# Kernel optimization log

Hardware: AMD Instinct MI355X
Metric: run time of the kernel (lower is better)

The kernel has to match this reference:

```python
import jax, jax.numpy as jnp
import numpy as np

WS = 4          # window_size
NH = 4          # num_heads
HID = 192       # hidden_dim
IN_DIM = 64     # input_dim
GROUPS = 8      # min(8, hidden_dim)
EPS = 1e-5


def layer_norm(x, g, b):
    mu = jnp.mean(x, axis=-1, keepdims=True)
    var = jnp.var(x, axis=-1, keepdims=True)
    return (x - mu) * jax.lax.rsqrt(var + EPS) * g + b


def group_norm(x, g, b):
    # x: [B, C, H, W], groups over channels
    B, C, H, W = x.shape
    xg = x.reshape(B, GROUPS, C // GROUPS, H, W)
    mu = jnp.mean(xg, axis=(2, 3, 4), keepdims=True)
    var = jnp.var(xg, axis=(2, 3, 4), keepdims=True)
    xn = ((xg - mu) * jax.lax.rsqrt(var + EPS)).reshape(B, C, H, W)
    return xn * g[None, :, None, None] + b[None, :, None, None]


def setup_inputs() -> dict:
    key = jax.random.key(0)
    ks = jax.random.split(key, 16)
    B, H, W = 8, 128, 128
    s = lambda *shape: 0.02
    inp = {
        "x": jax.random.normal(ks[0], (B, IN_DIM, H, W), jnp.float32),
        "h": jax.random.normal(ks[1], (B, HID, H, W), jnp.float32),
        "c": jax.random.normal(ks[2], (B, HID, H, W), jnp.float32),
        # in_proj: Conv2d(input_dim+hidden_dim -> hidden_dim, 1x1)
        "w_in": jax.random.normal(ks[3], (HID, IN_DIM + HID), jnp.float32) * 0.02,
        "b_in": jnp.zeros((HID,), jnp.float32),
        # LocalWindowAttention params
        "ln_g": jnp.ones((HID,), jnp.float32),
        "ln_b": jnp.zeros((HID,), jnp.float32),
        "w_qkv": jax.random.normal(ks[4], (3 * HID, HID), jnp.float32) * 0.02,
        "b_qkv": jnp.zeros((3 * HID,), jnp.float32),
        "w_proj": jax.random.normal(ks[5], (HID, HID), jnp.float32) * 0.02,
        "b_proj": jnp.zeros((HID,), jnp.float32),
        # GroupNorm (shared: applied to attn_map and hnext)
        "gn_g": jnp.ones((HID,), jnp.float32),
        "gn_b": jnp.zeros((HID,), jnp.float32),
        # gates_conv: Conv2d(hidden_dim -> 4*hidden_dim, 1x1)
        "w_gates": jax.random.normal(ks[6], (4 * HID, HID), jnp.float32) * 0.02,
        "b_gates": jnp.zeros((4 * HID,), jnp.float32),
    }
    return inp


def reference(x, h, c, w_in, b_in, ln_g, ln_b, w_qkv, b_qkv,
              w_proj, b_proj, gn_g, gn_b, w_gates, b_gates):
    B, _, H, W = x.shape
    C = HID
    hd = C // NH
    scale = hd ** -0.5

    # in_proj (1x1 conv == channel GEMM)
    comb = jnp.concatenate([x, h], axis=1)
    proj = jnp.einsum('oc,bchw->bohw', w_in, comb) + b_in[None, :, None, None]

    # H, W are multiples of WS -> no reflect padding (matches torch common path)
    nh, nw = H // WS, W // WS
    # window_partition: [B, C, H, W] -> [B*nh*nw, WS*WS, C]
    xw = proj.reshape(B, C, nh, WS, nw, WS).transpose(0, 2, 4, 3, 5, 1)
    xw = xw.reshape(B * nh * nw, WS * WS, C)

    # LocalWindowAttention
    xn = layer_norm(xw, ln_g, ln_b)
    qkv = xn @ w_qkv.T + b_qkv                       # [Bw, N, 3C]
    Bw, N, _ = qkv.shape
    qkv = qkv.reshape(Bw, N, 3, NH, hd)
    q = qkv[:, :, 0].transpose(0, 2, 1, 3)           # [Bw, NH, N, hd]
    k = qkv[:, :, 1].transpose(0, 2, 1, 3)
    v = qkv[:, :, 2].transpose(0, 2, 1, 3)
    attn = jax.nn.softmax(jnp.einsum('bhnd,bhmd->bhnm', q, k) * scale, axis=-1)
    out = jnp.einsum('bhnm,bhmd->bhnd', attn, v)
    out = out.transpose(0, 2, 1, 3).reshape(Bw, N, C)
    out = out @ w_proj.T + b_proj

    # window_unpartition: [B*nh*nw, WS*WS, C] -> [B, C, H, W]
    amap = out.reshape(B, nh, nw, WS, WS, C).transpose(0, 5, 1, 3, 2, 4)
    amap = amap.reshape(B, C, H, W)

    amap = group_norm(amap, gn_g, gn_b)

    # gates (1x1 conv) + LSTM cell math
    gates = jnp.einsum('oc,bchw->bohw', w_gates, amap) + b_gates[None, :, None, None]
    ci, cf, co, cg = jnp.split(gates, 4, axis=1)
    i = jax.nn.sigmoid(ci)
    f = jax.nn.sigmoid(cf)
    o = jax.nn.sigmoid(co)
    g = jnp.tanh(cg)
    cnext = f * c + i * g
    hnext = o * jnp.tanh(cnext)
    hnext = group_norm(hnext, gn_g, gn_b)
    return (hnext, cnext)
```

## Files before the change

kernel.cpp:

```cpp
#include <hip/hip_runtime.h>

#define HW 16384
#define W_IMG 128
#define CH 192
#define CIN 64
#define P_TOT 131072
#define EPS 1e-5f

__device__ __forceinline__ void blockReduce2(float& a, float& b2, float* lds) {
#pragma unroll
  for (int off = 32; off > 0; off >>= 1) {
    a  += __shfl_down(a,  off, 64);
    b2 += __shfl_down(b2, off, 64);
  }
  int wv = threadIdx.x >> 6, ln = threadIdx.x & 63;
  if (ln == 0) { lds[wv] = a; lds[4 + wv] = b2; }
  __syncthreads();
  if (threadIdx.x == 0) {
    a  = lds[0] + lds[1] + lds[2] + lds[3];
    b2 = lds[4] + lds[5] + lds[6] + lds[7];
  }
}

__global__ __launch_bounds__(256) void k0_prep(
    const float* __restrict__ w_g, float* __restrict__ wT)
{
  int idx = blockIdx.x * 256 + threadIdx.x;
  if (idx < 147456) {
    int row = idx / 192, c = idx - row * 192;
    wT[(size_t)c * 768 + row] = w_g[idx];
  }
}

__global__ __launch_bounds__(256) void k3_fused(
    const float* __restrict__ x,  const float* __restrict__ h,
    const float* __restrict__ w_in, const float* __restrict__ b_in,
    const float* __restrict__ ln_g, const float* __restrict__ ln_b,
    const float* __restrict__ w_qkv, const float* __restrict__ b_qkv,
    const float* __restrict__ w_proj, const float* __restrict__ b_proj,
    float* __restrict__ amap)
{
  __shared__ float buf[576 * 16];
  __shared__ float xnb[192 * 16];
  __shared__ float sc[4 * 16 * 16];
  __shared__ float mu_s[16], rs_s[16];
  const int tid = threadIdx.x;
  const int wid = blockIdx.x;
  const int b  = wid >> 10;
  const int wy = (wid >> 5) & 31;
  const int wx = wid & 31;
  const int pix0 = (wy * 4) * W_IMG + wx * 4;

  for (int idx = tid; idx < 1024; idx += 256) {
    int cch = idx >> 2, ty = idx & 3;
    const float* src = (cch < 64)
        ? x + (size_t)(b * CIN + cch) * HW + pix0 + ty * W_IMG
        : h + (size_t)(b * CH + (cch - 64)) * HW + pix0 + ty * W_IMG;
    const float4 v = *(const float4*)src;
    float* d = &buf[cch * 16 + ty * 4];
    d[0] = v.x; d[1] = v.y; d[2] = v.z; d[3] = v.w;
  }
  __syncthreads();

  if (tid < 192) {
    const int j = tid;
    float acc[16];
    float bj = b_in[j];
#pragma unroll
    for (int t = 0; t < 16; ++t) acc[t] = bj;
    const float* wr = w_in + (size_t)j * 256;
#pragma unroll 4
    for (int c = 0; c < 256; ++c) {
      float wv = wr[c];
      const float* xr = &buf[c * 16];
#pragma unroll
      for (int t = 0; t < 16; ++t) acc[t] = fmaf(wv, xr[t], acc[t]);
    }
    float* o = &xnb[j * 16];
#pragma unroll
    for (int t = 0; t < 16; ++t) o[t] = acc[t];
  }
  __syncthreads();

  if (tid < 16) {
    float s = 0.f, s2 = 0.f;
    for (int j = 0; j < 192; ++j) { float v = xnb[j * 16 + tid]; s += v; s2 += v * v; }
    float mu = s * (1.f / 192.f);
    float var = s2 * (1.f / 192.f) - mu * mu;
    mu_s[tid] = mu;
    rs_s[tid] = rsqrtf(fmaxf(var, 0.f) + EPS);
  }
  __syncthreads();

  for (int idx = tid; idx < 3072; idx += 256) {
    int j = idx >> 4, t = idx & 15;
    xnb[idx] = (xnb[idx] - mu_s[t]) * rs_s[t] * ln_g[j] + ln_b[j];
  }
  __syncthreads();

  for (int j = tid; j < 576; j += 256) {
    float acc[16];
    float bj = b_qkv[j];
#pragma unroll
    for (int t = 0; t < 16; ++t) acc[t] = bj;
    const float* wr = w_qkv + (size_t)j * 192;
#pragma unroll 4
    for (int c = 0; c < 192; ++c) {
      float wv = wr[c];
      const float* xr = &xnb[c * 16];
#pragma unroll
      for (int t = 0; t < 16; ++t) acc[t] = fmaf(wv, xr[t], acc[t]);
    }
    float* qr = &buf[j * 16];
#pragma unroll
    for (int t = 0; t < 16; ++t) qr[t] = acc[t];
  }
  __syncthreads();

  const float scale = 0.14433756729740643f;
  for (int q = tid; q < 1024; q += 256) {
    int hh = q >> 8, t1 = (q >> 4) & 15, t2 = q & 15;
    const float* qq = &buf[(hh * 48) * 16 + t1];
    const float* kk = &buf[(192 + hh * 48) * 16 + t2];
    float sv = 0.f;
#pragma unroll
    for (int d = 0; d < 48; ++d) sv = fmaf(qq[d * 16], kk[d * 16], sv);
    sc[q] = sv * scale;
  }
  __syncthreads();

  if (tid < 64) {
    float* row = &sc[tid * 16];
    float m = row[0];
#pragma unroll
    for (int t = 1; t < 16; ++t) m = fmaxf(m, row[t]);
    float sum = 0.f;
#pragma unroll
    for (int t = 0; t < 16; ++t) { float e = __expf(row[t] - m); row[t] = e; sum += e; }
    float inv = 1.f / sum;
#pragma unroll
    for (int t = 0; t < 16; ++t) row[t] *= inv;
  }
  __syncthreads();

  for (int rnd = 0; rnd < 12; ++rnd) {
    int q = rnd * 256 + tid;
    int cc = q >> 4, t = q & 15;
    const float* pr = &sc[(cc / 48) * 256 + t * 16];
    const float* vr = &buf[(384 + cc) * 16];
    float sv = 0.f;
#pragma unroll
    for (int t2 = 0; t2 < 16; ++t2) sv = fmaf(pr[t2], vr[t2], sv);
    xnb[cc * 16 + t] = sv;
  }
  __syncthreads();

  if (tid < 192) {
    const int o = tid;
    float acc[16];
    float bo = b_proj[o];
#pragma unroll
    for (int t = 0; t < 16; ++t) acc[t] = bo;
    const float* wr = w_proj + (size_t)o * 192;
#pragma unroll 4
    for (int c = 0; c < 192; ++c) {
      float wv = wr[c];
      const float* xr = &xnb[c * 16];
#pragma unroll
      for (int t = 0; t < 16; ++t) acc[t] = fmaf(wv, xr[t], acc[t]);
    }
    float* op = amap + (size_t)(b * CH + o) * HW + pix0;
#pragma unroll
    for (int ty = 0; ty < 4; ++ty) {
      *(float4*)(op + ty * W_IMG) =
          make_float4(acc[ty * 4], acc[ty * 4 + 1], acc[ty * 4 + 2], acc[ty * 4 + 3]);
    }
  }
}

__global__ __launch_bounds__(256) void k4_stats(
    const float* __restrict__ src, float* __restrict__ stats)
{
  __shared__ float lds[8];
  int blk = blockIdx.x;
  int chunk = blk & 15, bc = blk >> 4;
  int b = bc / 192, cch = bc % 192;
  const float4 v = *(const float4*)(src + (size_t)bc * HW + chunk * 1024 + threadIdx.x * 4);
  float s  = v.x + v.y + v.z + v.w;
  float s2 = v.x * v.x + v.y * v.y + v.z * v.z + v.w * v.w;
  blockReduce2(s, s2, lds);
  if (threadIdx.x == 0) {
    atomicAdd(&stats[(b * 8 + cch / 24) * 2],     s);
    atomicAdd(&stats[(b * 8 + cch / 24) * 2 + 1], s2);
  }
}

__global__ __launch_bounds__(256) void k4b_scale(
    const float* __restrict__ stats, const float* __restrict__ gn_g,
    const float* __restrict__ gn_b, float* __restrict__ scaleS, float* __restrict__ shiftS)
{
  int idx = blockIdx.x * 256 + threadIdx.x;
  if (idx >= 1536) return;
  int b = idx / 192, cch = idx % 192, g = cch / 24;
  float n = 24.f * HW;
  float mu  = stats[(b * 8 + g) * 2] / n;
  float var = stats[(b * 8 + g) * 2 + 1] / n - mu * mu;
  float rs = rsqrtf(fmaxf(var, 0.f) + EPS);
  float scl = rs * gn_g[cch];
  scaleS[idx] = scl;
  shiftS[idx] = gn_b[cch] - mu * scl;
}

__global__ __launch_bounds__(256) void k6_gates(
    float* __restrict__ outp,
    const float* __restrict__ wT,
    const float* __restrict__ b_g, const float* __restrict__ cin,
    const float* __restrict__ scaleS, const float* __restrict__ shiftS)
{
  __shared__ float tile[192 * 64];
  const int tid = threadIdx.x;
  const int b  = blockIdx.x >> 8;
  const int s0 = (blockIdx.x & 255) * 64;
  float* cout = outp + (size_t)P_TOT * CH;

  for (int idx = tid; idx < 12288; idx += 256) {
    int c = idx >> 6, p = idx & 63;
    float raw = outp[(size_t)(b * CH + c) * HW + s0 + p];
    tile[idx] = fmaf(raw, scaleS[b * CH + c], shiftS[b * CH + c]);
  }
  __syncthreads();

  const int lane = tid & 63;
  const int wv = __builtin_amdgcn_readfirstlane(tid >> 6);

  for (int jg = wv * 6; jg < wv * 6 + 6; ++jg) {
    const int j0 = jg * 8;
    float acc[32];
#pragma unroll
    for (int k = 0; k < 4; ++k)
#pragma unroll
      for (int r = 0; r < 8; ++r) acc[k * 8 + r] = b_g[k * 192 + j0 + r];
#pragma unroll 2
    for (int c = 0; c < 192; ++c) {
      float a = tile[c * 64 + lane];
      const float* wc = wT + (size_t)c * 768 + j0;
#pragma unroll
      for (int k = 0; k < 4; ++k)
#pragma unroll
        for (int r = 0; r < 8; ++r)
          acc[k * 8 + r] = fmaf(a, wc[k * 192 + r], acc[k * 8 + r]);
    }
#pragma unroll
    for (int r = 0; r < 8; ++r) {
      size_t base = (size_t)(b * CH + j0 + r) * HW + s0 + lane;
      float ci = acc[r], cf = acc[8 + r], co = acc[16 + r], cg = acc[24 + r];
      float iv = 1.f / (1.f + __expf(-ci));
      float fv = 1.f / (1.f + __expf(-cf));
      float ov = 1.f / (1.f + __expf(-co));
      float gv = 1.f - 2.f / (__expf(2.f * cg) + 1.f);
      float cn = fmaf(fv, cin[base], iv * gv);
      cout[base] = cn;
      float th = 1.f - 2.f / (__expf(2.f * cn) + 1.f);
      outp[base] = ov * th;
    }
  }
}

__global__ __launch_bounds__(256) void k7_hnext(
    const float* __restrict__ stats2,
    const float* __restrict__ gn_g, const float* __restrict__ gn_b,
    float* __restrict__ outp)
{
  int blk = blockIdx.x;
  int chunk = blk & 15, bc = blk >> 4;
  int b = bc / 192, cch = bc % 192, g = cch / 24;
  float n = 24.f * HW;
  float mu  = stats2[(b * 8 + g) * 2] / n;
  float var = stats2[(b * 8 + g) * 2 + 1] / n - mu * mu;
  float rs = rsqrtf(fmaxf(var, 0.f) + EPS);
  float scl = rs * gn_g[cch];
  float shf = gn_b[cch] - mu * scl;
  float* p = outp + (size_t)bc * HW + chunk * 1024 + threadIdx.x * 4;
  float4 v = *(float4*)p;
  v.x = fmaf(v.x, scl, shf); v.y = fmaf(v.y, scl, shf);
  v.z = fmaf(v.z, scl, shf); v.w = fmaf(v.w, scl, shf);
  *(float4*)p = v;
}

extern "C" void kernel_launch(void* const* d_in, const int* in_sizes, int n_in,
                              void* d_out, int out_size, void* d_ws, size_t ws_size,
                              hipStream_t stream) {
  (void)in_sizes; (void)n_in; (void)out_size; (void)ws_size;
  const float* x      = (const float*)d_in[0];
  const float* h      = (const float*)d_in[1];
  const float* c      = (const float*)d_in[2];
  const float* w_in   = (const float*)d_in[3];
  const float* b_in   = (const float*)d_in[4];
  const float* ln_g   = (const float*)d_in[5];
  const float* ln_b   = (const float*)d_in[6];
  const float* w_qkv  = (const float*)d_in[7];
  const float* b_qkv  = (const float*)d_in[8];
  const float* w_proj = (const float*)d_in[9];
  const float* b_proj = (const float*)d_in[10];
  const float* gn_g   = (const float*)d_in[11];
  const float* gn_b   = (const float*)d_in[12];
  const float* w_g    = (const float*)d_in[13];
  const float* b_g    = (const float*)d_in[14];
  float* outp = (float*)d_out;
  char* ws = (char*)d_ws;
  float* wT     = (float*)ws;
  float* statsA = (float*)(ws + 589824);
  float* stats2 = (float*)(ws + 590336);
  float* scaleS = (float*)(ws + 590848);
  float* shiftS = (float*)(ws + 596992);

  hipMemsetAsync(statsA, 0, 1024, stream);

  k0_prep  <<<576, 256, 0, stream>>>(w_g, wT);
  k3_fused <<<8192, 256, 0, stream>>>(x, h, w_in, b_in, ln_g, ln_b,
                                      w_qkv, b_qkv, w_proj, b_proj, outp);
  k4_stats <<<24576, 256, 0, stream>>>(outp, statsA);
  k4b_scale<<<6, 256, 0, stream>>>(statsA, gn_g, gn_b, scaleS, shiftS);
  k6_gates <<<2048, 256, 0, stream>>>(outp, wT, b_g, c, scaleS, shiftS);
  k4_stats <<<24576, 256, 0, stream>>>(outp, stats2);
  k7_hnext <<<24576, 256, 0, stream>>>(stats2, gn_g, gn_b, outp);
}
```

Before: 3.177 ms.

## Transpose attention weights and spread fused window matmuls over all threads

Pre-transposes w_in, w_qkv and w_proj in the prep kernel so that neighbouring threads read neighbouring weight addresses. The fused window-attention kernel now has every thread compute four pixels for one output channel, instead of 192 threads each computing sixteen. The aim is to use all 256 threads, coalesce the weight loads and reduce register pressure. It also parallelises the layernorm statistics and the softmax (using shuffles over a padded score buffer). In exchange, each thread re-reads the weights once per quarter-window, the prep kernel does more transpose work, and the workspace grows.

Measured after the change: 4.195 ms. 32.1% more time.

```diff
diff --git a/kernel.cpp b/kernel.cpp
--- a/kernel.cpp
+++ b/kernel.cpp
@@ -23,27 +23,38 @@
 }
 
 __global__ __launch_bounds__(256) void k0_prep(
-    const float* __restrict__ w_g, float* __restrict__ wT)
+    const float* __restrict__ w_in, const float* __restrict__ w_qkv,
+    const float* __restrict__ w_proj, const float* __restrict__ w_g,
+    float* __restrict__ wTin, float* __restrict__ wTqkv,
+    float* __restrict__ wTproj, float* __restrict__ wTg)
 {
   int idx = blockIdx.x * 256 + threadIdx.x;
-  if (idx < 147456) {
-    int row = idx / 192, c = idx - row * 192;
-    wT[(size_t)c * 768 + row] = w_g[idx];
+  if (idx < 49152) {
+    int j = idx >> 8, c = idx & 255;
+    wTin[c * 192 + j] = w_in[idx];
+  } else if (idx < 159744) {
+    int t = idx - 49152; int j = t / 192, c = t - j * 192;
+    wTqkv[c * 576 + j] = w_qkv[t];
+  } else if (idx < 196608) {
+    int t = idx - 159744; int o = t / 192, c = t - o * 192;
+    wTproj[c * 192 + o] = w_proj[t];
+  } else if (idx < 344064) {
+    int t = idx - 196608; int row = t / 192, c = t - row * 192;
+    wTg[c * 768 + row] = w_g[t];
   }
 }
 
 __global__ __launch_bounds__(256) void k3_fused(
     const float* __restrict__ x,  const float* __restrict__ h,
-    const float* __restrict__ w_in, const float* __restrict__ b_in,
+    const float* __restrict__ wTin, const float* __restrict__ b_in,
     const float* __restrict__ ln_g, const float* __restrict__ ln_b,
-    const float* __restrict__ w_qkv, const float* __restrict__ b_qkv,
-    const float* __restrict__ w_proj, const float* __restrict__ b_proj,
+    const float* __restrict__ wTqkv, const float* __restrict__ b_qkv,
+    const float* __restrict__ wTproj, const float* __restrict__ b_proj,
     float* __restrict__ amap)
 {
-  __shared__ float buf[576 * 16];
-  __shared__ float xnb[192 * 16];
-  __shared__ float sc[4 * 16 * 16];
-  __shared__ float mu_s[16], rs_s[16];
+  __shared__ float buf[9216];
+  __shared__ float xnb[3072];
+  __shared__ float scb[1088];
   const int tid = threadIdx.x;
   const int wid = blockIdx.x;
   const int b  = wid >> 10;
@@ -62,91 +73,108 @@
   }
   __syncthreads();
 
-  if (tid < 192) {
-    const int j = tid;
-    float acc[16];
+  for (int r = 0; r < 3; ++r) {
+    int idx = r * 256 + tid;
+    int j = idx >> 2, q = idx & 3;
     float bj = b_in[j];
-#pragma unroll
-    for (int t = 0; t < 16; ++t) acc[t] = bj;
-    const float* wr = w_in + (size_t)j * 256;
+    float a0 = bj, a1 = bj, a2 = bj, a3 = bj;
+    const float* xr = &buf[q * 4];
+    const float* wp = wTin + j;
 #pragma unroll 4
     for (int c = 0; c < 256; ++c) {
-      float wv = wr[c];
-      const float* xr = &buf[c * 16];
-#pragma unroll
-      for (int t = 0; t < 16; ++t) acc[t] = fmaf(wv, xr[t], acc[t]);
-    }
-    float* o = &xnb[j * 16];
-#pragma unroll
-    for (int t = 0; t < 16; ++t) o[t] = acc[t];
-  }
-  __syncthreads();
-
+      float wv = wp[c * 192];
+      const float* xc = xr + c * 16;
+      a0 = fmaf(wv, xc[0], a0);
+      a1 = fmaf(wv, xc[1], a1);
+      a2 = fmaf(wv, xc[2], a2);
+      a3 = fmaf(wv, xc[3], a3);
+    }
+    float* o = &xnb[j * 16 + q * 4];
+    o[0] = a0; o[1] = a1; o[2] = a2; o[3] = a3;
+  }
+  __syncthreads();
+
+  {
+    int g = tid >> 4, t = tid & 15;
+    float s = 0.f, s2 = 0.f;
+    const float* p = &xnb[g * 12 * 16 + t];
+#pragma unroll
+    for (int jj = 0; jj < 12; ++jj) { float v = p[jj * 16]; s += v; s2 = fmaf(v, v, s2); }
+    scb[tid] = s; scb[256 + tid] = s2;
+  }
+  __syncthreads();
   if (tid < 16) {
     float s = 0.f, s2 = 0.f;
-    for (int j = 0; j < 192; ++j) { float v = xnb[j * 16 + tid]; s += v; s2 += v * v; }
+#pragma unroll
+    for (int g = 0; g < 16; ++g) { s += scb[g * 16 + tid]; s2 += scb[256 + g * 16 + tid]; }
     float mu = s * (1.f / 192.f);
     float var = s2 * (1.f / 192.f) - mu * mu;
-    mu_s[tid] = mu;
-    rs_s[tid] = rsqrtf(fmaxf(var, 0.f) + EPS);
+    scb[512 + tid] = mu;
+    scb[528 + tid] = rsqrtf(fmaxf(var, 0.f) + EPS);
   }
   __syncthreads();
 
   for (int idx = tid; idx < 3072; idx += 256) {
     int j = idx >> 4, t = idx & 15;
-    xnb[idx] = (xnb[idx] - mu_s[t]) * rs_s[t] * ln_g[j] + ln_b[j];
-  }
-  __syncthreads();
-
-  for (int j = tid; j < 576; j += 256) {
-    float acc[16];
+    xnb[idx] = (xnb[idx] - scb[512 + t]) * scb[528 + t] * ln_g[j] + ln_b[j];
+  }
+  __syncthreads();
+
+  for (int r = 0; r < 9; ++r) {
+    int idx = r * 256 + tid;
+    int j = idx >> 2, q = idx & 3;
     float bj = b_qkv[j];
-#pragma unroll
-    for (int t = 0; t < 16; ++t) acc[t] = bj;
-    const float* wr = w_qkv + (size_t)j * 192;
+    float a0 = bj, a1 = bj, a2 = bj, a3 = bj;
+    const float* xr = &xnb[q * 4];
+    const float* wp = wTqkv + j;
 #pragma unroll 4
     for (int c = 0; c < 192; ++c) {
-      float wv = wr[c];
-      const float* xr = &xnb[c * 16];
-#pragma unroll
-      for (int t = 0; t < 16; ++t) acc[t] = fmaf(wv, xr[t], acc[t]);
-    }
-    float* qr = &buf[j * 16];
-#pragma unroll
-    for (int t = 0; t < 16; ++t) qr[t] = acc[t];
+      float wv = wp[c * 576];
+      const float* xc = xr + c * 16;
+      a0 = fmaf(wv, xc[0], a0);
+      a1 = fmaf(wv, xc[1], a1);
+      a2 = fmaf(wv, xc[2], a2);
+      a3 = fmaf(wv, xc[3], a3);
+    }
+    float* o = &buf[j * 16 + q * 4];
+    o[0] = a0; o[1] = a1; o[2] = a2; o[3] = a3;
   }
   __syncthreads();
 
   const float scale = 0.14433756729740643f;
-  for (int q = tid; q < 1024; q += 256) {
-    int hh = q >> 8, t1 = (q >> 4) & 15, t2 = q & 15;
+  for (int r = 0; r < 4; ++r) {
+    int idx = r * 256 + tid;
+    int hh = idx >> 8, t1 = (idx >> 4) & 15, t2 = idx & 15;
     const float* qq = &buf[(hh * 48) * 16 + t1];
     const float* kk = &buf[(192 + hh * 48) * 16 + t2];
     float sv = 0.f;
 #pragma unroll
     for (int d = 0; d < 48; ++d) sv = fmaf(qq[d * 16], kk[d * 16], sv);
-    sc[q] = sv * scale;
-  }
-  __syncthreads();
-
-  if (tid < 64) {
-    float* row = &sc[tid * 16];
-    float m = row[0];
-#pragma unroll
-    for (int t = 1; t < 16; ++t) m = fmaxf(m, row[t]);
-    float sum = 0.f;
-#pragma unroll
-    for (int t = 0; t < 16; ++t) { float e = __expf(row[t] - m); row[t] = e; sum += e; }
-    float inv = 1.f / sum;
-#pragma unroll
-    for (int t = 0; t < 16; ++t) row[t] *= inv;
-  }
-  __syncthreads();
-
-  for (int rnd = 0; rnd < 12; ++rnd) {
-    int q = rnd * 256 + tid;
-    int cc = q >> 4, t = q & 15;
-    const float* pr = &sc[(cc / 48) * 256 + t * 16];
+    scb[(hh * 16 + t1) * 17 + t2] = sv * scale;
+  }
+  __syncthreads();
+
+  {
+    int rrow = tid >> 2, i = tid & 3;
+    float* row = &scb[rrow * 17 + i * 4];
+    float v0 = row[0], v1 = row[1], v2 = row[2], v3 = row[3];
+    float m = fmaxf(fmaxf(v0, v1), fmaxf(v2, v3));
+    m = fmaxf(m, __shfl_xor(m, 1));
+    m = fmaxf(m, __shfl_xor(m, 2));
+    float e0 = __expf(v0 - m), e1 = __expf(v1 - m);
+    float e2 = __expf(v2 - m), e3 = __expf(v3 - m);
+    float s = e0 + e1 + e2 + e3;
+    s += __shfl_xor(s, 1);
+    s += __shfl_xor(s, 2);
+    float inv = 1.f / s;
+    row[0] = e0 * inv; row[1] = e1 * inv; row[2] = e2 * inv; row[3] = e3 * inv;
+  }
+  __syncthreads();
+
+  for (int r = 0; r < 12; ++r) {
+    int idx = r * 256 + tid;
+    int cc = idx >> 4, t = idx & 15;
+    const float* pr = &scb[((cc / 48) * 16 + t) * 17];
     const float* vr = &buf[(384 + cc) * 16];
     float sv = 0.f;
 #pragma unroll
@@ -155,26 +183,24 @@
   }
   __syncthreads();
 
-  if (tid < 192) {
-    const int o = tid;
-    float acc[16];
+  for (int r = 0; r < 3; ++r) {
+    int idx = r * 256 + tid;
+    int o = idx >> 2, q = idx & 3;
     float bo = b_proj[o];
-#pragma unroll
-    for (int t = 0; t < 16; ++t) acc[t] = bo;
-    const float* wr = w_proj + (size_t)o * 192;
+    float a0 = bo, a1 = bo, a2 = bo, a3 = bo;
+    const float* xr = &xnb[q * 4];
+    const float* wp = wTproj + o;
 #pragma unroll 4
     for (int c = 0; c < 192; ++c) {
-      float wv = wr[c];
-      const float* xr = &xnb[c * 16];
-#pragma unroll
-      for (int t = 0; t < 16; ++t) acc[t] = fmaf(wv, xr[t], acc[t]);
-    }
-    float* op = amap + (size_t)(b * CH + o) * HW + pix0;
-#pragma unroll
-    for (int ty = 0; ty < 4; ++ty) {
-      *(float4*)(op + ty * W_IMG) =
-          make_float4(acc[ty * 4], acc[ty * 4 + 1], acc[ty * 4 + 2], acc[ty * 4 + 3]);
-    }
+      float wv = wp[c * 192];
+      const float* xc = xr + c * 16;
+      a0 = fmaf(wv, xc[0], a0);
+      a1 = fmaf(wv, xc[1], a1);
+      a2 = fmaf(wv, xc[2], a2);
+      a3 = fmaf(wv, xc[3], a3);
+    }
+    float* op = amap + (size_t)(b * CH + o) * HW + pix0 + q * W_IMG;
+    *(float4*)op = make_float4(a0, a1, a2, a3);
   }
 }
 
@@ -308,20 +334,24 @@
   const float* b_g    = (const float*)d_in[14];
   float* outp = (float*)d_out;
   char* ws = (char*)d_ws;
-  float* wT     = (float*)ws;
-  float* statsA = (float*)(ws + 589824);
-  float* stats2 = (float*)(ws + 590336);
-  float* scaleS = (float*)(ws + 590848);
-  float* shiftS = (float*)(ws + 596992);
+  float* wTin   = (float*)ws;
+  float* wTqkv  = (float*)(ws + 196608);
+  float* wTproj = (float*)(ws + 638976);
+  float* wTg    = (float*)(ws + 786432);
+  float* statsA = (float*)(ws + 1376256);
+  float* stats2 = (float*)(ws + 1376768);
+  float* scaleS = (float*)(ws + 1377280);
+  float* shiftS = (float*)(ws + 1383424);
 
   hipMemsetAsync(statsA, 0, 1024, stream);
 
-  k0_prep  <<<576, 256, 0, stream>>>(w_g, wT);
-  k3_fused <<<8192, 256, 0, stream>>>(x, h, w_in, b_in, ln_g, ln_b,
-                                      w_qkv, b_qkv, w_proj, b_proj, outp);
+  k0_prep  <<<1344, 256, 0, stream>>>(w_in, w_qkv, w_proj, w_g,
+                                      wTin, wTqkv, wTproj, wTg);
+  k3_fused <<<8192, 256, 0, stream>>>(x, h, wTin, b_in, ln_g, ln_b,
+                                      wTqkv, b_qkv, wTproj, b_proj, outp);
   k4_stats <<<24576, 256, 0, stream>>>(outp, statsA);
   k4b_scale<<<6, 256, 0, stream>>>(statsA, gn_g, gn_b, scaleS, shiftS);
-  k6_gates <<<2048, 256, 0, stream>>>(outp, wT, b_g, c, scaleS, shiftS);
+  k6_gates <<<2048, 256, 0, stream>>>(outp, wTg, b_g, c, scaleS, shiftS);
   k4_stats <<<24576, 256, 0, stream>>>(outp, stats2);
   k7_hnext <<<24576, 256, 0, stream>>>(stats2, gn_g, gn_b, outp);
 }
```

## Shrink LDS footprint in fused attention kernel and parallelize reductions

Applied to the files above, without the earlier changes.

Cuts shared memory per block from about 50KB to about 39KB by computing Q/K first, doing scores and softmax in two head-pairs through a small scratch buffer, storing probabilities over the Q region, then computing V into the freed K region. The QKV projection for Q/K now uses all 256 threads with 8 pixels each instead of 3 uneven rounds, LayerNorm statistics use a two-level reduction over all threads, and softmax uses 4 lanes per row with shuffles plus padded rows. The goal is higher occupancy and less serialized work, at the cost of extra barriers and a separate V projection pass.

New measurement: 3.205 ms. About the same (+0.9%).

```diff
diff --git a/kernel.cpp b/kernel.cpp
--- a/kernel.cpp
+++ b/kernel.cpp
@@ -40,10 +40,9 @@
     const float* __restrict__ w_proj, const float* __restrict__ b_proj,
     float* __restrict__ amap)
 {
-  __shared__ float buf[576 * 16];
-  __shared__ float xnb[192 * 16];
-  __shared__ float sc[4 * 16 * 16];
-  __shared__ float mu_s[16], rs_s[16];
+  __shared__ float qk[6144];
+  __shared__ float xnb[3072];
+  __shared__ float scr[544];
   const int tid = threadIdx.x;
   const int wid = blockIdx.x;
   const int b  = wid >> 10;
@@ -57,7 +56,7 @@
         ? x + (size_t)(b * CIN + cch) * HW + pix0 + ty * W_IMG
         : h + (size_t)(b * CH + (cch - 64)) * HW + pix0 + ty * W_IMG;
     const float4 v = *(const float4*)src;
-    float* d = &buf[cch * 16 + ty * 4];
+    float* d = &qk[cch * 16 + ty * 4];
     d[0] = v.x; d[1] = v.y; d[2] = v.z; d[3] = v.w;
   }
   __syncthreads();
@@ -72,7 +71,7 @@
 #pragma unroll 4
     for (int c = 0; c < 256; ++c) {
       float wv = wr[c];
-      const float* xr = &buf[c * 16];
+      const float* xr = &qk[c * 16];
 #pragma unroll
       for (int t = 0; t < 16; ++t) acc[t] = fmaf(wv, xr[t], acc[t]);
     }
@@ -82,28 +81,95 @@
   }
   __syncthreads();
 
+  {
+    int g = tid >> 4, t = tid & 15;
+    float s = 0.f, s2 = 0.f;
+    const float* p = &xnb[g * 12 * 16 + t];
+#pragma unroll
+    for (int jj = 0; jj < 12; ++jj) { float v = p[jj * 16]; s += v; s2 = fmaf(v, v, s2); }
+    scr[tid] = s; scr[256 + tid] = s2;
+  }
+  __syncthreads();
   if (tid < 16) {
     float s = 0.f, s2 = 0.f;
-    for (int j = 0; j < 192; ++j) { float v = xnb[j * 16 + tid]; s += v; s2 += v * v; }
+#pragma unroll
+    for (int g = 0; g < 16; ++g) { s += scr[g * 16 + tid]; s2 += scr[256 + g * 16 + tid]; }
     float mu = s * (1.f / 192.f);
     float var = s2 * (1.f / 192.f) - mu * mu;
-    mu_s[tid] = mu;
-    rs_s[tid] = rsqrtf(fmaxf(var, 0.f) + EPS);
+    scr[512 + tid] = mu;
+    scr[528 + tid] = rsqrtf(fmaxf(var, 0.f) + EPS);
   }
   __syncthreads();
 
   for (int idx = tid; idx < 3072; idx += 256) {
     int j = idx >> 4, t = idx & 15;
-    xnb[idx] = (xnb[idx] - mu_s[t]) * rs_s[t] * ln_g[j] + ln_b[j];
-  }
-  __syncthreads();
-
-  for (int j = tid; j < 576; j += 256) {
+    xnb[idx] = (xnb[idx] - scr[512 + t]) * scr[528 + t] * ln_g[j] + ln_b[j];
+  }
+  __syncthreads();
+
+  for (int r = 0; r < 3; ++r) {
+    int idx = r * 256 + tid;
+    int j = idx >> 1, th = idx & 1;
+    float bj = b_qkv[j];
+    float acc[8];
+#pragma unroll
+    for (int i = 0; i < 8; ++i) acc[i] = bj;
+    const float* wr = w_qkv + (size_t)j * 192;
+    const float* xr = &xnb[th * 8];
+#pragma unroll 4
+    for (int c = 0; c < 192; ++c) {
+      float wv = wr[c];
+      const float* xc = xr + c * 16;
+#pragma unroll
+      for (int i = 0; i < 8; ++i) acc[i] = fmaf(wv, xc[i], acc[i]);
+    }
+    float* o = &qk[j * 16 + th * 8];
+#pragma unroll
+    for (int i = 0; i < 8; ++i) o[i] = acc[i];
+  }
+  __syncthreads();
+
+  const float scale = 0.14433756729740643f;
+#pragma unroll
+  for (int p = 0; p < 2; ++p) {
+    for (int r = 0; r < 2; ++r) {
+      int idx = r * 256 + tid;
+      int hhl = idx >> 8, t1 = (idx >> 4) & 15, t2 = idx & 15;
+      int hh = 2 * p + hhl;
+      const float* qq = &qk[(hh * 48) * 16 + t1];
+      const float* kk = &qk[3072 + (hh * 48) * 16 + t2];
+      float sv = 0.f;
+#pragma unroll
+      for (int d = 0; d < 48; ++d) sv = fmaf(qq[d * 16], kk[d * 16], sv);
+      scr[(hhl * 16 + t1) * 17 + t2] = sv * scale;
+    }
+    __syncthreads();
+    if (tid < 128) {
+      int rrow = tid >> 2, i = tid & 3;
+      const float* row = &scr[rrow * 17 + i * 4];
+      float v0 = row[0], v1 = row[1], v2 = row[2], v3 = row[3];
+      float m = fmaxf(fmaxf(v0, v1), fmaxf(v2, v3));
+      m = fmaxf(m, __shfl_xor(m, 1));
+      m = fmaxf(m, __shfl_xor(m, 2));
+      float e0 = __expf(v0 - m), e1 = __expf(v1 - m);
+      float e2 = __expf(v2 - m), e3 = __expf(v3 - m);
+      float s = e0 + e1 + e2 + e3;
+      s += __shfl_xor(s, 1);
+      s += __shfl_xor(s, 2);
+      float inv = 1.f / s;
+      float* pd = &qk[(p * 32 + rrow) * 17 + i * 4];
+      pd[0] = e0 * inv; pd[1] = e1 * inv; pd[2] = e2 * inv; pd[3] = e3 * inv;
+    }
+    __syncthreads();
+  }
+
+  if (tid < 192) {
+    const int j = tid;
     float acc[16];
-    float bj = b_qkv[j];
+    float bj = b_qkv[384 + j];
 #pragma unroll
     for (int t = 0; t < 16; ++t) acc[t] = bj;
-    const float* wr = w_qkv + (size_t)j * 192;
+    const float* wr = w_qkv + (size_t)(384 + j) * 192;
 #pragma unroll 4
     for (int c = 0; c < 192; ++c) {
       float wv = wr[c];
@@ -111,43 +177,17 @@
 #pragma unroll
       for (int t = 0; t < 16; ++t) acc[t] = fmaf(wv, xr[t], acc[t]);
     }
-    float* qr = &buf[j * 16];
-#pragma unroll
-    for (int t = 0; t < 16; ++t) qr[t] = acc[t];
-  }
-  __syncthreads();
-
-  const float scale = 0.14433756729740643f;
-  for (int q = tid; q < 1024; q += 256) {
-    int hh = q >> 8, t1 = (q >> 4) & 15, t2 = q & 15;
-    const float* qq = &buf[(hh * 48) * 16 + t1];
-    const float* kk = &buf[(192 + hh * 48) * 16 + t2];
-    float sv = 0.f;
-#pragma unroll
-    for (int d = 0; d < 48; ++d) sv = fmaf(qq[d * 16], kk[d * 16], sv);
-    sc[q] = sv * scale;
-  }
-  __syncthreads();
-
-  if (tid < 64) {
-    float* row = &sc[tid * 16];
-    float m = row[0];
-#pragma unroll
-    for (int t = 1; t < 16; ++t) m = fmaxf(m, row[t]);
-    float sum = 0.f;
-#pragma unroll
-    for (int t = 0; t < 16; ++t) { float e = __expf(row[t] - m); row[t] = e; sum += e; }
-    float inv = 1.f / sum;
-#pragma unroll
-    for (int t = 0; t < 16; ++t) row[t] *= inv;
-  }
-  __syncthreads();
-
-  for (int rnd = 0; rnd < 12; ++rnd) {
-    int q = rnd * 256 + tid;
-    int cc = q >> 4, t = q & 15;
-    const float* pr = &sc[(cc / 48) * 256 + t * 16];
-    const float* vr = &buf[(384 + cc) * 16];
+    float* o = &qk[3072 + j * 16];
+#pragma unroll
+    for (int t = 0; t < 16; ++t) o[t] = acc[t];
+  }
+  __syncthreads();
+
+  for (int r = 0; r < 12; ++r) {
+    int idx = r * 256 + tid;
+    int cc = idx >> 4, t = idx & 15;
+    const float* pr = &qk[((cc / 48) * 16 + t) * 17];
+    const float* vr = &qk[3072 + cc * 16];
     float sv = 0.f;
 #pragma unroll
     for (int t2 = 0; t2 < 16; ++t2) sv = fmaf(pr[t2], vr[t2], sv);
```
